# Kernel optimization log

Hardware: AMD Instinct MI355X
Metric: run time of the kernel (lower is better)

Reference implementation:

```python
import jax, jax.numpy as jnp
import numpy as np

EMB_SIZE = 768
BLOCK_SIZE = 64
OFFSET = 1  # bert cls offset


def setup_inputs() -> dict:
    key = jax.random.key(0)
    ks = jax.random.split(key, 10)
    n, c, d, h, E, M, P = 4, 1024, 768, 12, 42, 8, 1024
    sequence_output = jax.random.normal(ks[0], (n, c, d), jnp.float32)
    attention = jax.random.uniform(ks[1], (n, h, c, c), jnp.float32)
    attention = attention / attention.sum(-1, keepdims=True)  # softmax-like rows
    Wh = jax.random.normal(ks[2], (EMB_SIZE, 2 * d), jnp.float32) * 0.02
    bh = jax.random.normal(ks[3], (EMB_SIZE,), jnp.float32) * 0.02
    Wt = jax.random.normal(ks[4], (EMB_SIZE, 2 * d), jnp.float32) * 0.02
    bt = jax.random.normal(ks[5], (EMB_SIZE,), jnp.float32) * 0.02
    Wb = jax.random.normal(ks[6], (99, EMB_SIZE * BLOCK_SIZE), jnp.float32) * 0.02
    mention_pos = jax.random.randint(ks[7], (n, E, M), 0, c - 1 - OFFSET, jnp.int32)
    mention_mask = jax.random.randint(ks[8], (n, E, M), 0, 2, jnp.int32)
    mention_mask = mention_mask.at[:, :, 0].set(1)  # every entity has >=1 mention
    hts = jax.random.randint(ks[9], (n, P, 2), 0, E, jnp.int32)
    return {"sequence_output": sequence_output, "attention": attention,
            "Wh": Wh, "bh": bh, "Wt": Wt, "bt": bt, "Wb": Wb,
            "mention_pos": mention_pos, "mention_mask": mention_mask, "hts": hts}


def _get_hrt_doc(seq, att, pos, mask, ht):
    # seq [c,d], att [h,c,c], pos/mask [E,M], ht [P,2]
    p = pos + OFFSET                                   # [E,M]
    valid = mask > 0
    memb = seq[p]                                      # [E,M,d] gather
    e_emb = jax.scipy.special.logsumexp(
        jnp.where(valid[..., None], memb, -jnp.inf), axis=1)  # [E,d]
    matt = att[:, p]                                   # [h,E,M,c] gather
    cnt = valid.sum(1).astype(seq.dtype)               # [E]
    e_att = (matt * valid[None, :, :, None].astype(seq.dtype)).sum(2)
    e_att = jnp.transpose(e_att, (1, 0, 2)) / cnt[:, None, None]  # [E,h,c] mention mean
    hs = e_emb[ht[:, 0]]                               # [P,d]
    ts = e_emb[ht[:, 1]]
    h_att = e_att[ht[:, 0]]                            # [P,h,c]
    t_att = e_att[ht[:, 1]]
    ht_att = (h_att * t_att).mean(1)                   # [P,c] head mean
    ht_att = ht_att / (ht_att.sum(1, keepdims=True) + 1e-5)
    rs = jnp.einsum('ld,rl->rd', seq, ht_att)          # [P,d]
    return hs, ts, rs


def reference(sequence_output, attention, Wh, bh, Wt, bt, Wb,
              mention_pos, mention_mask, hts):
    d = sequence_output.shape[-1]
    hs, ts, rs = jax.vmap(_get_hrt_doc)(sequence_output, attention,
                                        mention_pos, mention_mask, hts)
    hs = hs.reshape(-1, d)
    ts = ts.reshape(-1, d)
    rs = rs.reshape(-1, d)
    hs = jnp.tanh(jnp.concatenate([hs, rs], axis=1) @ Wh.T + bh)
    ts = jnp.tanh(jnp.concatenate([ts, rs], axis=1) @ Wt.T + bt)
    nb = EMB_SIZE // BLOCK_SIZE
    b1 = hs.reshape(-1, nb, BLOCK_SIZE)
    b2 = ts.reshape(-1, nb, BLOCK_SIZE)
    bl = (b1[:, :, :, None] * b2[:, :, None, :]).reshape(-1, EMB_SIZE * BLOCK_SIZE)
    logits = bl @ Wb.T                                 # [N, num_labels+2]
    return logits
```

## Files before the change

kernel.cpp:

```cpp
#include <hip/hip_runtime.h>
#include <hip/hip_bf16.h>
#include <hip/hip_fp16.h>
#include <math.h>

#define NDOC 4
#define CCC  1024
#define DDD  768
#define HHH  12
#define EEE  42
#define MMM  8
#define PPP  1024
#define NBQ  12
#define NK   99
#define NPAD 112

typedef __attribute__((ext_vector_type(8))) short short8v;
typedef __attribute__((ext_vector_type(8))) _Float16 half8;
typedef __attribute__((ext_vector_type(4))) float floatx4;

__device__ __forceinline__ unsigned short f32_to_bf16u(float f) {
  return __builtin_bit_cast(unsigned short, __float2bfloat16(f));
}
__device__ __forceinline__ unsigned short f32_to_f16u(float f) {
  return __builtin_bit_cast(unsigned short, __float2half(f));
}

__global__ __launch_bounds__(256) void k_eemb(const float* __restrict__ seq,
    const int* __restrict__ pos, const int* __restrict__ mask,
    unsigned short* __restrict__ eembB) {
  int e = blockIdx.x, doc = blockIdx.y;
  int base = (doc*EEE + e)*MMM;
  int p[MMM], mk[MMM];
#pragma unroll
  for (int m = 0; m < MMM; ++m) { p[m] = pos[base+m] + 1; mk[m] = mask[base+m]; }
  for (int d0 = threadIdx.x; d0 < DDD; d0 += 256) {
    float v[MMM]; float mx = -INFINITY;
#pragma unroll
    for (int m = 0; m < MMM; ++m) {
      v[m] = seq[(doc*CCC + p[m])*DDD + d0];
      if (mk[m]) mx = fmaxf(mx, v[m]);
    }
    float s = 0.f;
#pragma unroll
    for (int m = 0; m < MMM; ++m) if (mk[m]) s += expf(v[m]-mx);
    eembB[(doc*EEE + e)*DDD + d0] = f32_to_bf16u(logf(s) + mx);
  }
}

__global__ __launch_bounds__(256) void k_eatt(const float* __restrict__ att,
    const int* __restrict__ pos, const int* __restrict__ mask,
    float* __restrict__ eatt) {
  int head = blockIdx.x, e = blockIdx.y, doc = blockIdx.z;
  int base = (doc*EEE + e)*MMM;
  int j = threadIdx.x * 4;
  float ax=0.f, ay=0.f, az=0.f, aw=0.f; float cnt = 0.f;
#pragma unroll
  for (int m = 0; m < MMM; ++m) {
    int mk = mask[base+m];
    cnt += (float)mk;
    if (mk) {
      int pp = pos[base+m] + 1;
      const float4 a = *(const float4*)&att[((size_t)(doc*HHH + head)*CCC + pp)*CCC + j];
      ax += a.x; ay += a.y; az += a.z; aw += a.w;
    }
  }
  float inv = 1.f / cnt;
  float4 o; o.x = ax*inv; o.y = ay*inv; o.z = az*inv; o.w = aw*inv;
  *(float4*)&eatt[((size_t)((doc*EEE + e)*HHH + head))*CCC + j] = o;
}

__global__ __launch_bounds__(256) void k_htatt(const float* __restrict__ eatt,
    const int* __restrict__ hts, unsigned short* __restrict__ htB) {
  int b = blockIdx.x; int doc = b >> 10; int r = b & 1023;
  int h0 = hts[(doc*PPP + r)*2 + 0];
  int t0 = hts[(doc*PPP + r)*2 + 1];
  const float* ea0 = &eatt[(size_t)((doc*EEE + h0)*HHH)*CCC];
  const float* ea1 = &eatt[(size_t)((doc*EEE + t0)*HHH)*CCC];
  int j = threadIdx.x * 4;
  float vx=0.f, vy=0.f, vz=0.f, vw=0.f;
#pragma unroll
  for (int hh = 0; hh < HHH; ++hh) {
    const float4 a  = *(const float4*)&ea0[hh*CCC + j];
    const float4 bq = *(const float4*)&ea1[hh*CCC + j];
    vx += a.x*bq.x; vy += a.y*bq.y; vz += a.z*bq.z; vw += a.w*bq.w;
  }
  const float inv12 = 1.f/12.f;
  vx *= inv12; vy *= inv12; vz *= inv12; vw *= inv12;
  float part = vx + vy + vz + vw;
  __shared__ float red[4];
  for (int off = 32; off > 0; off >>= 1) part += __shfl_down(part, off, 64);
  int lane = threadIdx.x & 63, wv = threadIdx.x >> 6;
  if (lane == 0) red[wv] = part;
  __syncthreads();
  if (threadIdx.x == 0) red[0] = red[0]+red[1]+red[2]+red[3];
  __syncthreads();
  float sc = 1.f / (red[0] + 1e-5f);
  unsigned short o[4];
  o[0] = f32_to_bf16u(vx*sc); o[1] = f32_to_bf16u(vy*sc);
  o[2] = f32_to_bf16u(vz*sc); o[3] = f32_to_bf16u(vw*sc);
  *(uint2*)&htB[((size_t)(doc*PPP + r))*CCC + j] = *(const uint2*)o;
}

__global__ __launch_bounds__(256) void k_packW(const float* __restrict__ Wh,
    const float* __restrict__ Wt, unsigned short* __restrict__ WB) {
  int gid = blockIdx.x*256 + threadIdx.x;
  int half = gid >= 147456;
  int loc = half ? gid - 147456 : gid;
  const float* src = (half ? Wt : Wh) + (size_t)loc*8;
  float4 v0 = *(const float4*)src;
  float4 v1 = *(const float4*)(src+4);
  unsigned short o[8];
  o[0]=f32_to_bf16u(v0.x); o[1]=f32_to_bf16u(v0.y); o[2]=f32_to_bf16u(v0.z); o[3]=f32_to_bf16u(v0.w);
  o[4]=f32_to_bf16u(v1.x); o[5]=f32_to_bf16u(v1.y); o[6]=f32_to_bf16u(v1.z); o[7]=f32_to_bf16u(v1.w);
  *(uint4*)&WB[(size_t)half*1179648 + (size_t)loc*8] = *(const uint4*)o;
}

__global__ __launch_bounds__(256) void k_seqT(const float* __restrict__ seq,
    unsigned short* __restrict__ seqTB) {
  __shared__ float tl[64][65];
  int d0 = blockIdx.x * 64, c0 = blockIdx.y * 64, doc = blockIdx.z;
  int t = threadIdx.x;
#pragma unroll
  for (int rep = 0; rep < 4; ++rep) {
    int cr = rep*16 + (t >> 4);
    int d4 = (t & 15) * 4;
    float4 v = *(const float4*)&seq[((size_t)doc*CCC + c0 + cr)*DDD + d0 + d4];
    tl[cr][d4+0]=v.x; tl[cr][d4+1]=v.y; tl[cr][d4+2]=v.z; tl[cr][d4+3]=v.w;
  }
  __syncthreads();
#pragma unroll
  for (int rep = 0; rep < 4; ++rep) {
    int dr = rep*16 + (t >> 4);
    int c4 = (t & 15) * 4;
    unsigned short o[4];
#pragma unroll
    for (int kq = 0; kq < 4; ++kq)
      o[kq] = f32_to_bf16u(tl[c4+kq][dr]);
    *(uint2*)&seqTB[((size_t)doc*DDD + d0 + dr)*CCC + c0 + c4] = *(const uint2*)o;
  }
}

__global__ __launch_bounds__(256) void k_rs_mfma(
    const unsigned short* __restrict__ htB,
    const unsigned short* __restrict__ seqTB,
    unsigned short* __restrict__ rsB) {
  __shared__ unsigned short A_l[4096];
  __shared__ unsigned short B_l[4096];
  const int n0 = blockIdx.x * 128;
  const int m0 = blockIdx.y * 128;
  const int doc = m0 >> 10;
  const int mloc = m0 & 1023;
  const int t = threadIdx.x;
  const int lane = t & 63;
  const int ln = lane & 15, q4 = lane >> 4;
  const int w = t >> 6;
  const int wr = w >> 1, wc = w & 1;

  const int r0 = t >> 2;
  const int koff = (t & 3) * 8;
  const unsigned short* srcA0 = htB + ((size_t)doc*CCC + mloc + r0)*CCC + koff;
  const unsigned short* srcA1 = htB + ((size_t)doc*CCC + mloc + r0 + 64)*CCC + koff;
  const unsigned short* srcB0 = seqTB + ((size_t)doc*DDD + n0 + r0)*CCC + koff;
  const unsigned short* srcB1 = seqTB + ((size_t)doc*DDD + n0 + r0 + 64)*CCC + koff;

  floatx4 acc[4][4];
#pragma unroll
  for (int i = 0; i < 4; ++i)
#pragma unroll
    for (int j = 0; j < 4; ++j) acc[i][j] = (floatx4){0.f,0.f,0.f,0.f};

  for (int k0 = 0; k0 < CCC; k0 += 32) {
    uint4 va0 = *(const uint4*)(srcA0 + k0);
    uint4 va1 = *(const uint4*)(srcA1 + k0);
    uint4 vb0 = *(const uint4*)(srcB0 + k0);
    uint4 vb1 = *(const uint4*)(srcB1 + k0);
    __syncthreads();
    *(uint4*)&A_l[(size_t)t*8]       = va0;
    *(uint4*)&A_l[(size_t)(t+256)*8] = va1;
    *(uint4*)&B_l[(size_t)t*8]       = vb0;
    *(uint4*)&B_l[(size_t)(t+256)*8] = vb1;
    __syncthreads();
    short8v a[4], b[4];
#pragma unroll
    for (int rt = 0; rt < 4; ++rt)
      a[rt] = *(const short8v*)&A_l[((wr*64 + rt*16 + ln)*4 + q4)*8];
#pragma unroll
    for (int nt = 0; nt < 4; ++nt)
      b[nt] = *(const short8v*)&B_l[((wc*64 + nt*16 + ln)*4 + q4)*8];
#pragma unroll
    for (int rt = 0; rt < 4; ++rt)
#pragma unroll
      for (int nt = 0; nt < 4; ++nt)
        acc[rt][nt] = __builtin_amdgcn_mfma_f32_16x16x32_bf16(a[rt], b[nt], acc[rt][nt], 0, 0, 0);
  }
#pragma unroll
  for (int rt = 0; rt < 4; ++rt)
#pragma unroll
    for (int nt = 0; nt < 4; ++nt) {
      int col = n0 + wc*64 + nt*16 + ln;
#pragma unroll
      for (int reg = 0; reg < 4; ++reg) {
        int row = m0 + wr*64 + rt*16 + q4*4 + reg;
        rsB[(size_t)row*DDD + col] = f32_to_bf16u(acc[rt][nt][reg]);
      }
    }
}

__global__ __launch_bounds__(256) void k_heads_mfma(
    const unsigned short* __restrict__ eembB,
    const unsigned short* __restrict__ rsB,
    const int* __restrict__ hts,
    const unsigned short* __restrict__ WB,
    const float* __restrict__ bh, const float* __restrict__ bt,
    float* __restrict__ hsb, float* __restrict__ tsb) {
  __shared__ unsigned short A_l[4096];
  __shared__ unsigned short B_l[4096];
  const int which = blockIdx.z;
  const int n0 = blockIdx.x * 128;
  const int m0 = blockIdx.y * 128;
  const int doc = m0 >> 10;
  const int t = threadIdx.x;
  const int lane = t & 63;
  const int ln = lane & 15, q4 = lane >> 4;
  const int w = t >> 6;
  const int wr = w >> 1, wc = w & 1;

  const int r0 = t >> 2;
  const int koff = (t & 3) * 8;
  const int rgA0 = m0 + r0, rgA1 = m0 + r0 + 64;
  const int idx0 = hts[rgA0*2 + which];
  const int idx1 = hts[rgA1*2 + which];
  const unsigned short* srcE0 = eembB + (size_t)(doc*EEE + idx0)*DDD + koff;
  const unsigned short* srcE1 = eembB + (size_t)(doc*EEE + idx1)*DDD + koff;
  const unsigned short* srcR0 = rsB + (size_t)rgA0*DDD + koff;
  const unsigned short* srcR1 = rsB + (size_t)rgA1*DDD + koff;
  const unsigned short* WBz = WB + (size_t)which*1179648;
  const unsigned short* srcW0 = WBz + (size_t)(n0 + r0)*1536 + koff;
  const unsigned short* srcW1 = WBz + (size_t)(n0 + r0 + 64)*1536 + koff;

  floatx4 acc[4][4];
#pragma unroll
  for (int i = 0; i < 4; ++i)
#pragma unroll
    for (int j = 0; j < 4; ++j) acc[i][j] = (floatx4){0.f,0.f,0.f,0.f};

  for (int k0 = 0; k0 < 1536; k0 += 32) {
    uint4 va0 = (k0 < DDD) ? *(const uint4*)(srcE0 + k0) : *(const uint4*)(srcR0 + (k0 - DDD));
    uint4 va1 = (k0 < DDD) ? *(const uint4*)(srcE1 + k0) : *(const uint4*)(srcR1 + (k0 - DDD));
    uint4 vb0 = *(const uint4*)(srcW0 + k0);
    uint4 vb1 = *(const uint4*)(srcW1 + k0);
    __syncthreads();
    *(uint4*)&A_l[(size_t)t*8]       = va0;
    *(uint4*)&A_l[(size_t)(t+256)*8] = va1;
    *(uint4*)&B_l[(size_t)t*8]       = vb0;
    *(uint4*)&B_l[(size_t)(t+256)*8] = vb1;
    __syncthreads();
    short8v a[4], b[4];
#pragma unroll
    for (int rt = 0; rt < 4; ++rt)
      a[rt] = *(const short8v*)&A_l[((wr*64 + rt*16 + ln)*4 + q4)*8];
#pragma unroll
    for (int nt = 0; nt < 4; ++nt)
      b[nt] = *(const short8v*)&B_l[((wc*64 + nt*16 + ln)*4 + q4)*8];
#pragma unroll
    for (int rt = 0; rt < 4; ++rt)
#pragma unroll
      for (int nt = 0; nt < 4; ++nt)
        acc[rt][nt] = __builtin_amdgcn_mfma_f32_16x16x32_bf16(a[rt], b[nt], acc[rt][nt], 0, 0, 0);
  }
  const float* bias = which ? bt : bh;
  float* outp = which ? tsb : hsb;
#pragma unroll
  for (int rt = 0; rt < 4; ++rt)
#pragma unroll
    for (int nt = 0; nt < 4; ++nt) {
      int col = n0 + wc*64 + nt*16 + ln;
      float bsv = bias[col];
#pragma unroll
      for (int reg = 0; reg < 4; ++reg) {
        int row = m0 + wr*64 + rt*16 + q4*4 + reg;
        outp[(size_t)row*DDD + col] = tanhf(acc[rt][nt][reg] + bsv);
      }
    }
}

__global__ __launch_bounds__(256) void k_prep_w(const float* __restrict__ Wb,
    unsigned short* __restrict__ Wp) {
  int t = blockIdx.x*256 + threadIdx.x;
  int j8 = (t & 7) * 8;
  int n = (t >> 3) % NPAD;
  int ki = t / 896;
  unsigned short o[8];
  if (n < NK) {
    const float* src = &Wb[(size_t)n*49152 + ki*64 + j8];
    float4 v0 = *(const float4*)src;
    float4 v1 = *(const float4*)(src+4);
    o[0]=f32_to_f16u(v0.x); o[1]=f32_to_f16u(v0.y); o[2]=f32_to_f16u(v0.z); o[3]=f32_to_f16u(v0.w);
    o[4]=f32_to_f16u(v1.x); o[5]=f32_to_f16u(v1.y); o[6]=f32_to_f16u(v1.z); o[7]=f32_to_f16u(v1.w);
  } else {
#pragma unroll
    for (int e=0;e<8;++e) o[e]=0;
  }
  int js = (t & 7) >> 2, q = t & 3;
  int nt = n >> 4, lnn = n & 15;
  int c = ((js*7 + nt)*4 + q)*16 + lnn;
  *(uint4*)&Wp[(size_t)ki*7168 + c*8] = *(const uint4*)o;
}

__global__ __launch_bounds__(256) void k_pack_hs(const float* __restrict__ hs,
    unsigned short* __restrict__ hsT) {
  __shared__ float tl[64][65];
  int i0 = blockIdx.x * 64, r0 = blockIdx.y * 64;
  int t = threadIdx.x;
#pragma unroll
  for (int rep = 0; rep < 4; ++rep) {
    int r = rep*16 + (t >> 4);
    int c4 = (t & 15) * 4;
    float4 v = *(const float4*)&hs[(size_t)(r0 + r)*DDD + i0 + c4];
    tl[r][c4+0]=v.x; tl[r][c4+1]=v.y; tl[r][c4+2]=v.z; tl[r][c4+3]=v.w;
  }
  __syncthreads();
#pragma unroll
  for (int rep = 0; rep < 4; ++rep) {
    int i = rep*16 + (t >> 4);
    int r4 = (t & 15) * 4;
    unsigned short o[4];
#pragma unroll
    for (int kq = 0; kq < 4; ++kq)
      o[kq] = f32_to_f16u(tl[r4+kq][i]);
    *(uint2*)&hsT[(size_t)(i0 + i)*4096 + r0 + r4] = *(const uint2*)o;
  }
}

__global__ __launch_bounds__(128, 2) void k_logits_mfma(
    const unsigned short* __restrict__ hsT,
    const float* __restrict__ tsb,
    const unsigned short* __restrict__ Wp,
    unsigned short* __restrict__ P) {
  __shared__ unsigned short hsT_l[32*128];
  __shared__ unsigned short Bt_l[2*7168];
  const int slice = blockIdx.x;
  const int kbase = (slice >> 1)*64 + (slice & 1)*32;
  const int mtile = blockIdx.y;
  const int t = threadIdx.x;
  const int w = t >> 6;
  const int lane = t & 63;
  const int ln = lane & 15;
  const int q = lane >> 4;
  const int m0w = mtile*128 + w*64;

#pragma unroll
  for (int rep = 0; rep < 4; ++rep) {
    int c16 = t + rep*128;
    int ii = c16 >> 4;
    int c8 = (c16 & 15) * 8;
    uint4 v = *(const uint4*)&hsT[(size_t)(kbase + ii)*4096 + mtile*128 + c8];
    *(uint4*)&hsT_l[ii*128 + c8] = v;
  }

  __half2 tsr2[4][2][4];
  {
    int nb = kbase >> 6;
#pragma unroll
    for (int rt = 0; rt < 4; ++rt) {
      int row = m0w + rt*16 + ln;
#pragma unroll
      for (int js = 0; js < 2; ++js) {
        const float* p = &tsb[(size_t)row*DDD + nb*64 + js*32 + q*8];
        float4 v0 = *(const float4*)p;
        float4 v1 = *(const float4*)(p+4);
        tsr2[rt][js][0] = __floats2half2_rn(v0.x, v0.y);
        tsr2[rt][js][1] = __floats2half2_rn(v0.z, v0.w);
        tsr2[rt][js][2] = __floats2half2_rn(v1.x, v1.y);
        tsr2[rt][js][3] = __floats2half2_rn(v1.z, v1.w);
      }
    }
  }

  floatx4 acc[4][7];
#pragma unroll
  for (int rt = 0; rt < 4; ++rt)
#pragma unroll
    for (int nt = 0; nt < 7; ++nt)
      acc[rt][nt] = (floatx4){0.f,0.f,0.f,0.f};

  uint4 wreg[7];
#pragma unroll
  for (int r = 0; r < 7; ++r)
    wreg[r] = *(const uint4*)&Wp[(size_t)kbase*7168 + (t + r*128)*8];
#pragma unroll
  for (int r = 0; r < 7; ++r)
    *(uint4*)&Bt_l[(t + r*128)*8] = wreg[r];
  __syncthreads();

  for (int ii = 0; ii < 32; ++ii) {
    const unsigned short* bufc = Bt_l + (ii & 1)*7168;
    if (ii < 31) {
      int ki = kbase + ii + 1;
#pragma unroll
      for (int r = 0; r < 7; ++r)
        wreg[r] = *(const uint4*)&Wp[(size_t)ki*7168 + (t + r*128)*8];
    }
    __half2 hh[4];
#pragma unroll
    for (int rt = 0; rt < 4; ++rt) {
      unsigned short hb = hsT_l[ii*128 + w*64 + rt*16 + ln];
      hh[rt] = __half2half2(__ushort_as_half(hb));
    }
#pragma unroll
    for (int js = 0; js < 2; ++js) {
      half8 a[4];
#pragma unroll
      for (int rt = 0; rt < 4; ++rt) {
        uint4 au;
        au.x = __builtin_bit_cast(unsigned int, __hmul2(hh[rt], tsr2[rt][js][0]));
        au.y = __builtin_bit_cast(unsigned int, __hmul2(hh[rt], tsr2[rt][js][1]));
        au.z = __builtin_bit_cast(unsigned int, __hmul2(hh[rt], tsr2[rt][js][2]));
        au.w = __builtin_bit_cast(unsigned int, __hmul2(hh[rt], tsr2[rt][js][3]));
        a[rt] = __builtin_bit_cast(half8, au);
      }
#pragma unroll
      for (int nt = 0; nt < 7; ++nt) {
        half8 b = __builtin_bit_cast(half8,
            *(const short8v*)&bufc[((js*7 + nt)*4)*128 + lane*8]);
#pragma unroll
        for (int rt = 0; rt < 4; ++rt)
          acc[rt][nt] = __builtin_amdgcn_mfma_f32_16x16x32_f16(a[rt], b, acc[rt][nt], 0, 0, 0);
      }
    }
    if (ii < 31) {
      __syncthreads();
#pragma unroll
      for (int r = 0; r < 7; ++r)
        *(uint4*)&Bt_l[((ii+1) & 1)*7168 + (t + r*128)*8] = wreg[r];
      __syncthreads();
    }
  }

  unsigned short* Ps = P + (size_t)slice*(4096*NPAD);
#pragma unroll
  for (int nt = 0; nt < 7; ++nt) {
    int col = nt*16 + ln;
#pragma unroll
    for (int rt = 0; rt < 4; ++rt) {
#pragma unroll
      for (int reg = 0; reg < 4; ++reg) {
        int row = m0w + rt*16 + q*4 + reg;
        Ps[(size_t)row*NPAD + col] = f32_to_f16u(acc[rt][nt][reg]);
      }
    }
  }
}

__global__ __launch_bounds__(256) void k_logred(const unsigned short* __restrict__ P,
    float* __restrict__ out) {
  int idx = blockIdx.x*256 + threadIdx.x;
  int r = idx / NPAD;
  int c = idx % NPAD;
  if (c >= NK) return;
  float s = 0.f;
#pragma unroll
  for (int sl = 0; sl < 24; ++sl)
    s += __half2float(__ushort_as_half(P[(size_t)sl*(4096*NPAD) + idx]));
  out[(size_t)r*NK + c] = s;
}

extern "C" void kernel_launch(void* const* d_in, const int* in_sizes, int n_in,
                              void* d_out, int out_size, void* d_ws, size_t ws_size,
                              hipStream_t stream) {
  const float* seq  = (const float*)d_in[0];
  const float* att  = (const float*)d_in[1];
  const float* Wh   = (const float*)d_in[2];
  const float* bh   = (const float*)d_in[3];
  const float* Wt   = (const float*)d_in[4];
  const float* bt   = (const float*)d_in[5];
  const float* Wb   = (const float*)d_in[6];
  const int* pos    = (const int*)d_in[7];
  const int* mask   = (const int*)d_in[8];
  const int* hts    = (const int*)d_in[9];
  float* out = (float*)d_out;

  float* ws = (float*)d_ws;
  float*          eatt  = ws;
  unsigned short* htB   = (unsigned short*)(ws + 2064384);
  unsigned short* eembB = (unsigned short*)(ws + 4161536);
  unsigned short* seqTB = (unsigned short*)(ws + 4226048);
  unsigned short* WhtB  = (unsigned short*)(ws + 5798912);
  unsigned short* rsB   = (unsigned short*)(ws + 6978560);
  float*          hsb   = ws + 8551424;
  float*          tsb   = ws + 11697152;
  unsigned short* WpB   = (unsigned short*)eatt;
  unsigned short* hsTB  = (unsigned short*)seqTB;
  unsigned short* Pp    = (unsigned short*)(ws + 5798912);

  k_eemb<<<dim3(EEE, NDOC), 256, 0, stream>>>(seq, pos, mask, eembB);
  k_eatt<<<dim3(HHH, EEE, NDOC), 256, 0, stream>>>(att, pos, mask, eatt);
  k_htatt<<<dim3(NDOC*PPP), 256, 0, stream>>>(eatt, hts, htB);
  k_packW<<<dim3(1152), 256, 0, stream>>>(Wh, Wt, WhtB);
  k_seqT<<<dim3(DDD/64, CCC/64, NDOC), 256, 0, stream>>>(seq, seqTB);
  k_rs_mfma<<<dim3(6, 32), 256, 0, stream>>>(htB, seqTB, rsB);
  k_prep_w<<<dim3(2688), 256, 0, stream>>>(Wb, WpB);
  k_heads_mfma<<<dim3(6, 32, 2), 256, 0, stream>>>(eembB, rsB, hts, WhtB, bh, bt, hsb, tsb);
  k_pack_hs<<<dim3(DDD/64, 4096/64), 256, 0, stream>>>(hsb, hsTB);
  k_logits_mfma<<<dim3(24, 32), 128, 0, stream>>>(hsTB, tsb, WpB, Pp);
  k_logred<<<dim3(4096*NPAD/256), 256, 0, stream>>>(Pp, out);
}
```

Before: 221.8 us.

## Split logits K into 48 slices and load Wb fragments directly from global

The logits MFMA kernel now splits the K dimension into 48 slices of 16 rows each instead of 24 slices of 32, doubling the grid to improve CU occupancy. It also drops the double-buffered LDS staging of the packed Wb weights and their barriers, loading each B fragment straight from global memory (relying on L2 reuse across m-tiles). The partial-sum buffer moves to a new workspace offset to hold twice as many slices, and the reduction kernel sums 48 partials, which adds write/read traffic for the partial outputs.

After: 233.4 us. 5.2% more time.

```diff
diff --git a/kernel.cpp b/kernel.cpp
--- a/kernel.cpp
+++ b/kernel.cpp
@@ -13,6 +13,7 @@
 #define NBQ  12
 #define NK   99
 #define NPAD 112
+#define NSLICE 48
 
 typedef __attribute__((ext_vector_type(8))) short short8v;
 typedef __attribute__((ext_vector_type(8))) _Float16 half8;
@@ -332,15 +333,15 @@
   }
 }
 
-__global__ __launch_bounds__(128, 2) void k_logits_mfma(
+__global__ __launch_bounds__(128) void k_logits_mfma(
     const unsigned short* __restrict__ hsT,
     const float* __restrict__ tsb,
     const unsigned short* __restrict__ Wp,
     unsigned short* __restrict__ P) {
-  __shared__ unsigned short hsT_l[32*128];
-  __shared__ unsigned short Bt_l[2*7168];
+  __shared__ unsigned short hsT_l[16*128];
   const int slice = blockIdx.x;
-  const int kbase = (slice >> 1)*64 + (slice & 1)*32;
+  const int kbase = slice * 16;
+  const int nb = slice >> 2;
   const int mtile = blockIdx.y;
   const int t = threadIdx.x;
   const int w = t >> 6;
@@ -350,7 +351,7 @@
   const int m0w = mtile*128 + w*64;
 
 #pragma unroll
-  for (int rep = 0; rep < 4; ++rep) {
+  for (int rep = 0; rep < 2; ++rep) {
     int c16 = t + rep*128;
     int ii = c16 >> 4;
     int c8 = (c16 & 15) * 8;
@@ -359,21 +360,18 @@
   }
 
   __half2 tsr2[4][2][4];
-  {
-    int nb = kbase >> 6;
-#pragma unroll
-    for (int rt = 0; rt < 4; ++rt) {
-      int row = m0w + rt*16 + ln;
-#pragma unroll
-      for (int js = 0; js < 2; ++js) {
-        const float* p = &tsb[(size_t)row*DDD + nb*64 + js*32 + q*8];
-        float4 v0 = *(const float4*)p;
-        float4 v1 = *(const float4*)(p+4);
-        tsr2[rt][js][0] = __floats2half2_rn(v0.x, v0.y);
-        tsr2[rt][js][1] = __floats2half2_rn(v0.z, v0.w);
-        tsr2[rt][js][2] = __floats2half2_rn(v1.x, v1.y);
-        tsr2[rt][js][3] = __floats2half2_rn(v1.z, v1.w);
-      }
+#pragma unroll
+  for (int rt = 0; rt < 4; ++rt) {
+    int row = m0w + rt*16 + ln;
+#pragma unroll
+    for (int js = 0; js < 2; ++js) {
+      const float* p = &tsb[(size_t)row*DDD + nb*64 + js*32 + q*8];
+      float4 v0 = *(const float4*)p;
+      float4 v1 = *(const float4*)(p+4);
+      tsr2[rt][js][0] = __floats2half2_rn(v0.x, v0.y);
+      tsr2[rt][js][1] = __floats2half2_rn(v0.z, v0.w);
+      tsr2[rt][js][2] = __floats2half2_rn(v1.x, v1.y);
+      tsr2[rt][js][3] = __floats2half2_rn(v1.z, v1.w);
     }
   }
 
@@ -384,23 +382,10 @@
     for (int nt = 0; nt < 7; ++nt)
       acc[rt][nt] = (floatx4){0.f,0.f,0.f,0.f};
 
-  uint4 wreg[7];
-#pragma unroll
-  for (int r = 0; r < 7; ++r)
-    wreg[r] = *(const uint4*)&Wp[(size_t)kbase*7168 + (t + r*128)*8];
-#pragma unroll
-  for (int r = 0; r < 7; ++r)
-    *(uint4*)&Bt_l[(t + r*128)*8] = wreg[r];
   __syncthreads();
 
-  for (int ii = 0; ii < 32; ++ii) {
-    const unsigned short* bufc = Bt_l + (ii & 1)*7168;
-    if (ii < 31) {
-      int ki = kbase + ii + 1;
-#pragma unroll
-      for (int r = 0; r < 7; ++r)
-        wreg[r] = *(const uint4*)&Wp[(size_t)ki*7168 + (t + r*128)*8];
-    }
+  const unsigned short* wb = Wp + (size_t)kbase*7168;
+  for (int ii = 0; ii < 16; ++ii) {
     __half2 hh[4];
 #pragma unroll
     for (int rt = 0; rt < 4; ++rt) {
@@ -409,6 +394,11 @@
     }
 #pragma unroll
     for (int js = 0; js < 2; ++js) {
+      half8 b[7];
+#pragma unroll
+      for (int nt = 0; nt < 7; ++nt)
+        b[nt] = __builtin_bit_cast(half8,
+            *(const uint4*)&wb[((size_t)(js*7 + nt)*64 + lane)*8]);
       half8 a[4];
 #pragma unroll
       for (int rt = 0; rt < 4; ++rt) {
@@ -420,21 +410,12 @@
         a[rt] = __builtin_bit_cast(half8, au);
       }
 #pragma unroll
-      for (int nt = 0; nt < 7; ++nt) {
-        half8 b = __builtin_bit_cast(half8,
-            *(const short8v*)&bufc[((js*7 + nt)*4)*128 + lane*8]);
+      for (int nt = 0; nt < 7; ++nt)
 #pragma unroll
         for (int rt = 0; rt < 4; ++rt)
-          acc[rt][nt] = __builtin_amdgcn_mfma_f32_16x16x32_f16(a[rt], b, acc[rt][nt], 0, 0, 0);
-      }
-    }
-    if (ii < 31) {
-      __syncthreads();
-#pragma unroll
-      for (int r = 0; r < 7; ++r)
-        *(uint4*)&Bt_l[((ii+1) & 1)*7168 + (t + r*128)*8] = wreg[r];
-      __syncthreads();
-    }
+          acc[rt][nt] = __builtin_amdgcn_mfma_f32_16x16x32_f16(a[rt], b[nt], acc[rt][nt], 0, 0, 0);
+    }
+    wb += 7168;
   }
 
   unsigned short* Ps = P + (size_t)slice*(4096*NPAD);
@@ -460,7 +441,7 @@
   if (c >= NK) return;
   float s = 0.f;
 #pragma unroll
-  for (int sl = 0; sl < 24; ++sl)
+  for (int sl = 0; sl < NSLICE; ++sl)
     s += __half2float(__ushort_as_half(P[(size_t)sl*(4096*NPAD) + idx]));
   out[(size_t)r*NK + c] = s;
 }
@@ -491,7 +472,7 @@
   float*          tsb   = ws + 11697152;
   unsigned short* WpB   = (unsigned short*)eatt;
   unsigned short* hsTB  = (unsigned short*)seqTB;
-  unsigned short* Pp    = (unsigned short*)(ws + 5798912);
+  unsigned short* Pp    = (unsigned short*)(ws + 14842880);
 
   k_eemb<<<dim3(EEE, NDOC), 256, 0, stream>>>(seq, pos, mask, eembB);
   k_eatt<<<dim3(HHH, EEE, NDOC), 256, 0, stream>>>(att, pos, mask, eatt);
@@ -502,6 +483,6 @@
   k_prep_w<<<dim3(2688), 256, 0, stream>>>(Wb, WpB);
   k_heads_mfma<<<dim3(6, 32, 2), 256, 0, stream>>>(eembB, rsB, hts, WhtB, bh, bt, hsb, tsb);
   k_pack_hs<<<dim3(DDD/64, 4096/64), 256, 0, stream>>>(hsb, hsTB);
-  k_logits_mfma<<<dim3(24, 32), 128, 0, stream>>>(hsTB, tsb, WpB, Pp);
+  k_logits_mfma<<<dim3(NSLICE, 32), 128, 0, stream>>>(hsTB, tsb, WpB, Pp);
   k_logred<<<dim3(4096*NPAD/256), 256, 0, stream>>>(Pp, out);
 }
```
